# Kernel optimization log

Measured on AMD Instinct MI355X. Metric: run time of the kernel, lower is better.

## Reference

```python
import jax, jax.numpy as jnp
import numpy as np

C, FF, NH = 128, 2048, 8
B, D, H, W = 1, 16, 16, 16
EPS = 1e-5

def setup_inputs() -> dict:
    key = jax.random.key(0)
    ks = jax.random.split(key, 20)
    s = 0.02
    inp = {
        'x': jax.random.normal(ks[0], (B, C, D, H, W), jnp.float32),
        'Wq': jax.random.normal(ks[1], (C, C), jnp.float32) * s,
        'bq': jnp.zeros((C,), jnp.float32),
        'Wk': jax.random.normal(ks[2], (C, C), jnp.float32) * s,
        'bk': jnp.zeros((C,), jnp.float32),
        'Wv': jax.random.normal(ks[3], (C, C), jnp.float32) * s,
        'bv': jnp.zeros((C,), jnp.float32),
        'Wo': jax.random.normal(ks[4], (C, C), jnp.float32) * s,
        'bo': jnp.zeros((C,), jnp.float32),
        'W1': jax.random.normal(ks[5], (FF, C), jnp.float32) * s,
        'b1': jnp.zeros((FF,), jnp.float32),
        'W2': jax.random.normal(ks[6], (C, FF), jnp.float32) * s,
        'b2': jnp.zeros((C,), jnp.float32),
        'g1': jnp.ones((C,), jnp.float32),
        'be1': jnp.zeros((C,), jnp.float32),
        'g2': jnp.ones((C,), jnp.float32),
        'be2': jnp.zeros((C,), jnp.float32),
    }
    return inp

def _layernorm(t, g, b):
    # normalize over last (channel) dim, biased variance like torch LayerNorm
    m = jnp.mean(t, axis=-1, keepdims=True)
    v = jnp.mean(jnp.square(t - m), axis=-1, keepdims=True)
    return (t - m) * jax.lax.rsqrt(v + EPS) * g + b

def reference(x, Wq, bq, Wk, bk, Wv, bv, Wo, bo, W1, b1, W2, b2, g1, be1, g2, be2):
    b_, c, d, h, w = x.shape
    n = d * h * w
    hd = c // NH
    xf = x.reshape(b_, c, n)  # [B,C,N]
    # 1x1 conv3d == per-voxel linear over channels
    q = jnp.einsum('oc,bcn->bon', Wq, xf) + bq[:, None]
    k = jnp.einsum('oc,bcn->bon', Wk, xf) + bk[:, None]
    v = jnp.einsum('oc,bcn->bon', Wv, xf) + bv[:, None]
    q = q.reshape(b_, NH, hd, n)
    k = k.reshape(b_, NH, hd, n)
    v = v.reshape(b_, NH, hd, n)
    scores = jnp.einsum('bhcd,bhce->bhde', q, k) / (hd ** 0.5)  # [B,NH,N,N]
    probs = jax.nn.softmax(scores, axis=-1)
    attn = jnp.einsum('bhde,bhce->bhcd', probs, v).reshape(b_, c, n)
    attn = jnp.einsum('oc,bcn->bon', Wo, attn) + bo[:, None]
    x1 = xf + attn  # residual (dropout = identity at eval)
    x1 = _layernorm(x1.transpose(0, 2, 1), g1, be1)  # [B,N,C]
    hmid = jax.nn.relu(jnp.einsum('fc,bnc->bnf', W1, x1) + b1)
    ffn = jnp.einsum('cf,bnf->bnc', W2, hmid) + b2
    x2 = _layernorm(x1 + ffn, g2, be2)
    return x2.transpose(0, 2, 1).reshape(b_, c, d, h, w)
```

## Files before the change

### kernel.cpp

```cpp
#include <hip/hip_runtime.h>
#include <hip/hip_bf16.h>

typedef __hip_bfloat16 bf16;
typedef short short8 __attribute__((ext_vector_type(8)));
typedef float f32x4 __attribute__((ext_vector_type(4)));

#define C_   128
#define N_   4096
#define NH_  8
#define HD_  16
#define FF_  2048
#define SCALE_Q 0.360673760222241f

__device__ __forceinline__ unsigned short f2bf_bits(float f) {
    bf16 h = __float2bfloat16(f);
    return *reinterpret_cast<unsigned short*>(&h);
}
__device__ __forceinline__ unsigned int pack_trunc(float lo, float hi) {
    return (__float_as_uint(hi) & 0xffff0000u) | (__float_as_uint(lo) >> 16);
}
__device__ __forceinline__ short f2bf_trunc(float f) {
    return (short)(__float_as_uint(f) >> 16);
}
__device__ __forceinline__ float bfs2f(short s) {
    return __uint_as_float(((unsigned int)(unsigned short)s) << 16);
}
__device__ __forceinline__ float fast_exp2(float x) {
    return __builtin_amdgcn_exp2f(x);
}
__device__ __forceinline__ f32x4 mfma16(short8 a, short8 b, f32x4 c) {
    return __builtin_amdgcn_mfma_f32_16x16x32_bf16(a, b, c, 0, 0, 0);
}

__global__ void __launch_bounds__(256) k_prep(
    const float* __restrict__ Wq, const float* __restrict__ Wk,
    const float* __restrict__ Wv, const float* __restrict__ Wo,
    const float* __restrict__ W1, const float* __restrict__ W2,
    const float* __restrict__ x,
    bf16* __restrict__ Wqkvf, bf16* __restrict__ Wof,
    bf16* __restrict__ W1f, bf16* __restrict__ W2f,
    bf16* __restrict__ xTf)
{
    __shared__ float xs[4][512];
    const int tid = threadIdx.x, wave = tid >> 6, lane = tid & 63;
    const int gw = blockIdx.x * 4 + wave;
    const int q = lane >> 4;

    if (gw < 1152) {
        const float* src; bf16* dst; int K, otile, kch, blk;
        if (gw < 96)        { src = 0;  dst = Wqkvf; K = 128;  otile = gw >> 2;          kch = gw & 3;  blk = gw; }
        else if (gw < 128)  { int i = gw - 96;  src = Wo; dst = Wof;  K = 128;  otile = i >> 2; kch = i & 3;  blk = i; }
        else if (gw < 640)  { int i = gw - 128; src = W1; dst = W1f;  K = 128;  otile = i >> 2; kch = i & 3;  blk = i; }
        else                { int i = gw - 640; src = W2; dst = W2f;  K = 2048; otile = i >> 6; kch = i & 63; blk = i; }
        const int o = otile * 16 + (lane & 15);
        const int k0 = kch * 32 + 4 * q;
        const float* row;
        if (gw < 96) {
            row = (o < 128) ? (Wq + o * 128) : (o < 256) ? (Wk + (o - 128) * 128)
                                             : (Wv + (o - 256) * 128);
        } else {
            row = src + (size_t)o * K;
        }
        const float4 A = *(const float4*)(row + k0);
        const float4 B = *(const float4*)(row + k0 + 16);
        short8 v;
        v[0] = f2bf_bits(A.x); v[1] = f2bf_bits(B.x);
        v[2] = f2bf_bits(A.y); v[3] = f2bf_bits(B.y);
        v[4] = f2bf_bits(A.z); v[5] = f2bf_bits(B.z);
        v[6] = f2bf_bits(A.w); v[7] = f2bf_bits(B.w);
        *(short8*)((short*)dst + (size_t)blk * 512 + lane * 8) = v;
    } else {
        const int i = gw - 1152;
        const int n0 = (i >> 2) << 4, c0 = (i & 3) << 5;
        float* S = xs[wave];
        const int cl = lane & 31, ns = (lane >> 5) << 3;
        const float* p = x + (size_t)(c0 + cl) * N_ + n0 + ns;
        *(float4*)(S + cl * 16 + ns)     = *(const float4*)(p);
        *(float4*)(S + cl * 16 + ns + 4) = *(const float4*)(p + 4);
        short8 v;
        #pragma unroll
        for (int j = 0; j < 8; ++j) {
            const int ko = ((j & 1) << 4) + 4 * q + (j >> 1);
            v[j] = f2bf_bits(S[ko * 16 + (lane & 15)]);
        }
        *(short8*)((short*)xTf + (size_t)i * 512 + lane * 8) = v;
    }
}

__global__ void __launch_bounds__(256) k_qkv(
    const bf16* __restrict__ xTf, const bf16* __restrict__ Wqkvf,
    const float* __restrict__ bq, const float* __restrict__ bk, const float* __restrict__ bv,
    bf16* __restrict__ qf, bf16* __restrict__ kf, bf16* __restrict__ vf)
{
    __shared__ short tb[4][512];
    const int tid = threadIdx.x, wave = tid >> 6, lane = tid & 63;
    const int col = lane & 15, quad = lane >> 4;
    const int gw = blockIdx.x * 4 + wave;
    const int rt = gw / 24, ct = gw % 24;
    f32x4 acc = {};
    #pragma unroll
    for (int c = 0; c < 4; ++c) {
        short8 a = *(const short8*)(xTf + ((size_t)(rt * 4 + c) << 9) + lane * 8);
        short8 b = *(const short8*)(Wqkvf + ((size_t)(ct * 4 + c) << 9) + lane * 8);
        acc = mfma16(a, b, acc);
    }
    if (ct < 16) {
        short* T = tb[wave];
        const float bb = (ct < 8) ? bq[ct * 16 + col] : bk[(ct - 8) * 16 + col];
        const float sc = (ct < 8) ? SCALE_Q : 1.0f;
        #pragma unroll
        for (int r = 0; r < 4; ++r)
            T[(col >> 3) * 128 + (quad * 4 + r) * 8 + (col & 7)] =
                f2bf_trunc((acc[r] + bb) * sc);
        if (lane < 32) {
            short8 w = *(const short8*)(T + lane * 8);
            short* dst = (ct < 8) ? (short*)qf + ((ct << 8) + rt) * 256
                                  : (short*)kf + (((ct - 8) << 8) + rt) * 256;
            *(short8*)(dst + lane * 8) = w;
        }
    } else {
        const float bb = bv[(ct - 16) * 16 + col];
        short* vs = (short*)vf + ((((ct - 16) << 7) + (rt >> 1)) << 9);
        #pragma unroll
        for (int r = 0; r < 4; ++r) {
            const int local = quad * 4 + r;
            const int pos = local * 2 + (rt & 1);
            vs[((pos >> 3) * 16 + col) * 8 + (pos & 7)] = f2bf_trunc(acc[r] + bb);
        }
    }
}

__global__ void __launch_bounds__(256)
attn_kernel(const bf16* __restrict__ qf, const bf16* __restrict__ kf,
            const bf16* __restrict__ vf, bf16* __restrict__ af)
{
    __shared__ __align__(16) union {
        unsigned int P[4][2][320];
        float comb[4][64][8];
    } sh;
    const int tid = threadIdx.x, wave = tid >> 6, lane = tid & 63;
    const int col = lane & 15, quad = lane >> 4;
    const int gw = blockIdx.x;
    const int h  = gw >> 8;
    const int tile = gw & 255;
    const f32x4 zero = {};

    short8 aq = {};
    if (quad < 2)
        aq = *(const short8*)(qf + ((size_t)((h << 8) + tile) << 8) + lane * 8);

    f32x4 accO0 = {}, accO1 = {};
    float L[4] = {0.f, 0.f, 0.f, 0.f};

    const int kbeg = wave << 10;
    unsigned int* P0 = &sh.P[wave][0][0];
    unsigned int* P1 = &sh.P[wave][1][0];

    for (int i = 0; i < 32; i += 2) {
        const int mA = kbeg + (i << 5);
        const int mB = mA + 32;

        short8 bkA0 = {}, bkA1 = {}, bkB0 = {}, bkB1 = {};
        if (quad < 2) {
            const bf16* ka = kf + ((size_t)((h << 8) + (mA >> 4)) << 8) + lane * 8;
            bkA0 = *(const short8*)(ka);
            bkA1 = *(const short8*)(ka + 256);
            bkB0 = *(const short8*)(ka + 512);
            bkB1 = *(const short8*)(ka + 768);
        }
        f32x4 s0 = mfma16(aq, bkA0, zero);
        f32x4 s1 = mfma16(aq, bkA1, zero);
        f32x4 s2 = mfma16(aq, bkB0, zero);
        f32x4 s3 = mfma16(aq, bkB1, zero);
        #pragma unroll
        for (int r = 0; r < 4; ++r) {
            const float p0 = fast_exp2(s0[r]);
            const float p1 = fast_exp2(s1[r]);
            const float p2 = fast_exp2(s2[r]);
            const float p3 = fast_exp2(s3[r]);
            L[r] += (p0 + p1) + (p2 + p3);
            P0[(quad * 4 + r) * 20 + col] = pack_trunc(p0, p1);
            P1[(quad * 4 + r) * 20 + col] = pack_trunc(p2, p3);
        }
        short8 vA = *(const short8*)(vf + ((size_t)((h << 7) + (mA >> 5)) << 9) + lane * 8);
        short8 vB = *(const short8*)(vf + ((size_t)((h << 7) + (mB >> 5)) << 9) + lane * 8);
        short8 ap0 = *(const short8*)((const short*)P0 + col * 40 + quad * 8);
        accO0 = mfma16(ap0, vA, accO0);
        short8 ap1 = *(const short8*)((const short*)P1 + col * 40 + quad * 8);
        accO1 = mfma16(ap1, vB, accO1);
    }

    f32x4 accO;
    #pragma unroll
    for (int r = 0; r < 4; ++r) accO[r] = accO0[r] + accO1[r];

    __syncthreads();
    #pragma unroll
    for (int r = 0; r < 4; ++r) {
        sh.comb[wave][lane][r]     = accO[r];
        sh.comb[wave][lane][4 + r] = L[r];
    }
    __syncthreads();

    if (wave == 0) {
        #pragma unroll
        for (int r = 0; r < 4; ++r) {
            float O = sh.comb[0][lane][r] + sh.comb[1][lane][r]
                    + sh.comb[2][lane][r] + sh.comb[3][lane][r];
            float l = sh.comb[0][lane][4+r] + sh.comb[1][lane][4+r]
                    + sh.comb[2][lane][4+r] + sh.comb[3][lane][4+r];
            l += __shfl_xor(l, 1); l += __shfl_xor(l, 2);
            l += __shfl_xor(l, 4); l += __shfl_xor(l, 8);
            const int row16 = quad * 4 + r;
            const int pk = (col << 1) + (h & 1);
            af[((tile << 2) + (h >> 1)) * 512 + (((pk >> 3) << 4) + row16) * 8 + (pk & 7)] =
                __float2bfloat16(O / l);
        }
    }
}

__global__ void __launch_bounds__(256, 1)
k_mega(const bf16* __restrict__ af, const bf16* __restrict__ xTf,
       const bf16* __restrict__ Wof, const bf16* __restrict__ W1f, const bf16* __restrict__ W2f,
       const float* __restrict__ bo, const float* __restrict__ b1, const float* __restrict__ b2,
       const float* __restrict__ g1, const float* __restrict__ be1,
       const float* __restrict__ g2, const float* __restrict__ be2,
       float* __restrict__ out)
{
    __shared__ __align__(16) unsigned int Pb[4][2][320];
    __shared__ float comb[128][64];
    const int tid = threadIdx.x, wave = tid >> 6, lane = tid & 63;
    const int col = lane & 15, quad = lane >> 4;
    const int rt = blockIdx.x, n0 = rt << 4;
    const f32x4 zero = {};

    short8 ao[4], xt[4];
    #pragma unroll
    for (int c = 0; c < 4; ++c) {
        ao[c] = *(const short8*)(af  + ((size_t)(rt * 4 + c) << 9) + lane * 8);
        xt[c] = *(const short8*)(xTf + ((size_t)(rt * 4 + c) << 9) + lane * 8);
    }
    f32x4 d[8];
    #pragma unroll
    for (int t = 0; t < 8; ++t) d[t] = zero;
    short8 wa[4], wb[4];
    #pragma unroll
    for (int c = 0; c < 4; ++c)
        wa[c] = *(const short8*)(Wof + ((size_t)(c) << 9) + lane * 8);
    #pragma unroll
    for (int t = 0; t < 8; t += 2) {
        #pragma unroll
        for (int c = 0; c < 4; ++c)
            wb[c] = *(const short8*)(Wof + ((size_t)((t + 1) * 4 + c) << 9) + lane * 8);
        #pragma unroll
        for (int c = 0; c < 4; ++c) d[t] = mfma16(ao[c], wa[c], d[t]);
        if (t + 2 < 8) {
            #pragma unroll
            for (int c = 0; c < 4; ++c)
                wa[c] = *(const short8*)(Wof + ((size_t)((t + 2) * 4 + c) << 9) + lane * 8);
        }
        #pragma unroll
        for (int c = 0; c < 4; ++c) d[t + 1] = mfma16(ao[c], wb[c], d[t + 1]);
    }
    #pragma unroll
    for (int t = 0; t < 8; ++t) {
        const float bt = bo[t * 16 + col];
        #pragma unroll
        for (int r = 0; r < 4; ++r) d[t][r] += bt;
    }

    float x1f[4][8];
    #pragma unroll
    for (int c = 0; c < 4; ++c) {
        unsigned int* Pw = &Pb[wave][c & 1][0];
        const short* Ps = (const short*)Pw;
        #pragma unroll
        for (int r = 0; r < 4; ++r)
            Pw[(quad * 4 + r) * 20 + col] = pack_trunc(d[2 * c][r], d[2 * c + 1][r]);
        short8 ar = *(const short8*)(Ps + col * 40 + quad * 8);
        #pragma unroll
        for (int j = 0; j < 8; ++j)
            x1f[c][j] = bfs2f(ar[j]) + bfs2f(xt[c][j]);
    }

    float s = 0.f, ss = 0.f;
    #pragma unroll
    for (int c = 0; c < 4; ++c)
        #pragma unroll
        for (int j = 0; j < 8; ++j) { s += x1f[c][j]; ss += x1f[c][j] * x1f[c][j]; }
    s  += __shfl_xor(s, 16);  s  += __shfl_xor(s, 32);
    ss += __shfl_xor(ss, 16); ss += __shfl_xor(ss, 32);
    const float m1 = s * (1.f / 128.f);
    const float rstd1 = rsqrtf(ss * (1.f / 128.f) - m1 * m1 + 1e-5f);
    short8 aq1[4];
    #pragma unroll
    for (int c = 0; c < 4; ++c)
        #pragma unroll
        for (int j = 0; j < 8; ++j) {
            const int pos = quad * 8 + j;
            const int ko = ((pos & 1) << 4) + (pos >> 1);
            const int ch = c * 32 + ko;
            aq1[c][j] = f2bf_trunc((x1f[c][j] - m1) * rstd1 * g1[ch] + be1[ch]);
        }

    f32x4 ACC[8];
    #pragma unroll
    for (int t = 0; t < 8; ++t) ACC[t] = zero;
    const int fbase = wave << 4;
    short8 w1a[8], w2a[8], w1b[8], w2b[8];
    #pragma unroll
    for (int c = 0; c < 8; ++c) {
        w1a[c] = *(const short8*)(W1f + ((size_t)(fbase * 8 + c) << 9) + lane * 8);
        w2a[c] = *(const short8*)(W2f + ((size_t)(c * 64 + fbase) << 9) + lane * 8);
    }
    for (int i = 0; i < 16; i += 2) {
        const int f0 = fbase + i, f1 = f0 + 1;
        #pragma unroll
        for (int c = 0; c < 8; ++c) {
            w1b[c] = *(const short8*)(W1f + ((size_t)(f1 * 8 + c) << 9) + lane * 8);
            w2b[c] = *(const short8*)(W2f + ((size_t)(c * 64 + f1) << 9) + lane * 8);
        }
        {
            f32x4 p0 = zero, p1 = zero;
            #pragma unroll
            for (int c = 0; c < 4; ++c) p0 = mfma16(aq1[c], w1a[c], p0);
            #pragma unroll
            for (int c = 0; c < 4; ++c) p1 = mfma16(aq1[c], w1a[4 + c], p1);
            const float bb0 = b1[f0 * 32 + col], bb1 = b1[f0 * 32 + 16 + col];
            unsigned int* Pw = &Pb[wave][0][0];
            #pragma unroll
            for (int r = 0; r < 4; ++r)
                Pw[(quad * 4 + r) * 20 + col] =
                    pack_trunc(fmaxf(p0[r] + bb0, 0.f), fmaxf(p1[r] + bb1, 0.f));
            short8 ah = *(const short8*)((const short*)Pw + col * 40 + quad * 8);
            #pragma unroll
            for (int t = 0; t < 8; ++t) ACC[t] = mfma16(ah, w2a[t], ACC[t]);
        }
        if (i + 2 < 16) {
            const int f2 = f0 + 2;
            #pragma unroll
            for (int c = 0; c < 8; ++c) {
                w1a[c] = *(const short8*)(W1f + ((size_t)(f2 * 8 + c) << 9) + lane * 8);
                w2a[c] = *(const short8*)(W2f + ((size_t)(c * 64 + f2) << 9) + lane * 8);
            }
        }
        {
            f32x4 p0 = zero, p1 = zero;
            #pragma unroll
            for (int c = 0; c < 4; ++c) p0 = mfma16(aq1[c], w1b[c], p0);
            #pragma unroll
            for (int c = 0; c < 4; ++c) p1 = mfma16(aq1[c], w1b[4 + c], p1);
            const float bb0 = b1[f1 * 32 + col], bb1 = b1[f1 * 32 + 16 + col];
            unsigned int* Pw = &Pb[wave][1][0];
            #pragma unroll
            for (int r = 0; r < 4; ++r)
                Pw[(quad * 4 + r) * 20 + col] =
                    pack_trunc(fmaxf(p0[r] + bb0, 0.f), fmaxf(p1[r] + bb1, 0.f));
            short8 ah = *(const short8*)((const short*)Pw + col * 40 + quad * 8);
            #pragma unroll
            for (int t = 0; t < 8; ++t) ACC[t] = mfma16(ah, w2b[t], ACC[t]);
        }
    }

    #pragma unroll
    for (int t = 0; t < 8; ++t)
        #pragma unroll
        for (int r = 0; r < 4; ++r)
            comb[wave * 32 + t * 4 + r][lane] = ACC[t][r];
    if (wave == 0) {
        short* xb = (short*)&Pb[0][0][0];
        #pragma unroll
        for (int c = 0; c < 4; ++c)
            *(short8*)(xb + (col * 4 + c) * 32 + quad * 8) = aq1[c];
    }
    __syncthreads();

    {
        const short* xb = (const short*)&Pb[0][0][0];
        float t2[8][4];
        #pragma unroll
        for (int t = 0; t < 8; ++t) {
            const int ch = t * 16 + col;
            const int pk = (col << 1) + (t & 1);
            const int c = t >> 1;
            const float bb = b2[ch];
            #pragma unroll
            for (int r = 0; r < 4; ++r)
                t2[t][r] = comb[t * 4 + r][lane] + comb[32 + t * 4 + r][lane]
                         + comb[64 + t * 4 + r][lane] + comb[96 + t * 4 + r][lane]
                         + bb + bfs2f(xb[((quad * 4 + r) * 4 + c) * 32 + pk]);
        }
        #pragma unroll
        for (int r = 0; r < 4; ++r) {
            float S = 0.f, SS = 0.f;
            #pragma unroll
            for (int t = 0; t < 8; ++t) { S += t2[t][r]; SS += t2[t][r] * t2[t][r]; }
            S  += __shfl_xor(S, 1);  S  += __shfl_xor(S, 2);
            S  += __shfl_xor(S, 4);  S  += __shfl_xor(S, 8);
            SS += __shfl_xor(SS, 1); SS += __shfl_xor(SS, 2);
            SS += __shfl_xor(SS, 4); SS += __shfl_xor(SS, 8);
            const float m2 = S * (1.f / 128.f);
            const float rstd2 = rsqrtf(SS * (1.f / 128.f) - m2 * m2 + 1e-5f);
            #pragma unroll
            for (int tt = 0; tt < 2; ++tt) {
                const int t = wave * 2 + tt;
                const int ch = t * 16 + col;
                out[(size_t)ch * N_ + n0 + quad * 4 + r] =
                    (t2[t][r] - m2) * rstd2 * g2[ch] + be2[ch];
            }
        }
    }
}

extern "C" void kernel_launch(void* const* d_in, const int* in_sizes, int n_in,
                              void* d_out, int out_size, void* d_ws, size_t ws_size,
                              hipStream_t stream) {
    const float* x   = (const float*)d_in[0];
    const float* Wq  = (const float*)d_in[1];
    const float* bq  = (const float*)d_in[2];
    const float* Wk  = (const float*)d_in[3];
    const float* bk  = (const float*)d_in[4];
    const float* Wv  = (const float*)d_in[5];
    const float* bv  = (const float*)d_in[6];
    const float* Wo  = (const float*)d_in[7];
    const float* bo  = (const float*)d_in[8];
    const float* W1  = (const float*)d_in[9];
    const float* b1  = (const float*)d_in[10];
    const float* W2  = (const float*)d_in[11];
    const float* b2  = (const float*)d_in[12];
    const float* g1  = (const float*)d_in[13];
    const float* be1 = (const float*)d_in[14];
    const float* g2  = (const float*)d_in[15];
    const float* be2 = (const float*)d_in[16];
    float* out = (float*)d_out;

    char* ws = (char*)d_ws;
    bf16* xTf   = (bf16*)(ws + 0);
    bf16* qf    = (bf16*)(ws + 1048576);
    bf16* kf    = (bf16*)(ws + 2097152);
    bf16* vf    = (bf16*)(ws + 3145728);
    bf16* af    = (bf16*)(ws + 4194304);
    bf16* Wqkvf = (bf16*)(ws + 5242880);
    bf16* Wof   = (bf16*)(ws + 5341184);
    bf16* W1f   = (bf16*)(ws + 5373952);
    bf16* W2f   = (bf16*)(ws + 5898240);

    k_prep<<<544, 256, 0, stream>>>(Wq, Wk, Wv, Wo, W1, W2, x, Wqkvf, Wof, W1f, W2f, xTf);
    k_qkv<<<1536, 256, 0, stream>>>(xTf, Wqkvf, bq, bk, bv, qf, kf, vf);
    attn_kernel<<<2048, 256, 0, stream>>>(qf, kf, vf, af);
    k_mega<<<256, 256, 0, stream>>>(af, xTf, Wof, W1f, W2f, bo, b1, b2,
                                    g1, be1, g2, be2, out);
}
```

Baseline: 144.8 us.

## Process two query tiles per attention block to reuse K/V loads

Each attention block now handles two 16-row query tiles instead of one. Each K and V fragment loaded from global memory is used for both tiles, which halves K/V global traffic per query, and the grid shrinks from 2048 to 1024 blocks. The P scratch buffer is double-buffered by iteration parity, and two waves now finish the cross-wave combine instead of one. In exchange, each wave holds more registers and LDS, and there are half as many blocks to spread across CUs.

```diff
diff --git a/kernel.cpp b/kernel.cpp
--- a/kernel.cpp
+++ b/kernel.cpp
@@ -135,85 +135,85 @@
             const bf16* __restrict__ vf, bf16* __restrict__ af)
 {
     __shared__ __align__(16) union {
-        unsigned int P[4][2][320];
-        float comb[4][64][8];
+        unsigned int P[4][4][320];
+        float comb[4][64][16];
     } sh;
     const int tid = threadIdx.x, wave = tid >> 6, lane = tid & 63;
     const int col = lane & 15, quad = lane >> 4;
     const int gw = blockIdx.x;
-    const int h  = gw >> 8;
-    const int tile = gw & 255;
+    const int h  = gw >> 7;
+    const int tp = gw & 127;
+    const int t0 = tp << 1, t1 = t0 + 1;
     const f32x4 zero = {};
 
-    short8 aq = {};
-    if (quad < 2)
-        aq = *(const short8*)(qf + ((size_t)((h << 8) + tile) << 8) + lane * 8);
+    short8 aq0 = {}, aq1 = {};
+    if (quad < 2) {
+        aq0 = *(const short8*)(qf + ((size_t)((h << 8) + t0) << 8) + lane * 8);
+        aq1 = *(const short8*)(qf + ((size_t)((h << 8) + t1) << 8) + lane * 8);
+    }
 
     f32x4 accO0 = {}, accO1 = {};
-    float L[4] = {0.f, 0.f, 0.f, 0.f};
+    float L0[4] = {0.f, 0.f, 0.f, 0.f};
+    float L1[4] = {0.f, 0.f, 0.f, 0.f};
 
     const int kbeg = wave << 10;
-    unsigned int* P0 = &sh.P[wave][0][0];
-    unsigned int* P1 = &sh.P[wave][1][0];
-
-    for (int i = 0; i < 32; i += 2) {
-        const int mA = kbeg + (i << 5);
-        const int mB = mA + 32;
-
-        short8 bkA0 = {}, bkA1 = {}, bkB0 = {}, bkB1 = {};
+    for (int i = 0; i < 32; ++i) {
+        const int m0 = kbeg + (i << 5);
+        unsigned int* Pa = &sh.P[wave][(i & 1)][0];
+        unsigned int* Pb = &sh.P[wave][2 + (i & 1)][0];
+
+        short8 bk0 = {}, bk1 = {};
         if (quad < 2) {
-            const bf16* ka = kf + ((size_t)((h << 8) + (mA >> 4)) << 8) + lane * 8;
-            bkA0 = *(const short8*)(ka);
-            bkA1 = *(const short8*)(ka + 256);
-            bkB0 = *(const short8*)(ka + 512);
-            bkB1 = *(const short8*)(ka + 768);
-        }
-        f32x4 s0 = mfma16(aq, bkA0, zero);
-        f32x4 s1 = mfma16(aq, bkA1, zero);
-        f32x4 s2 = mfma16(aq, bkB0, zero);
-        f32x4 s3 = mfma16(aq, bkB1, zero);
+            const bf16* ka = kf + ((size_t)((h << 8) + (m0 >> 4)) << 8) + lane * 8;
+            bk0 = *(const short8*)(ka);
+            bk1 = *(const short8*)(ka + 256);
+        }
+        f32x4 sa0 = mfma16(aq0, bk0, zero);
+        f32x4 sa1 = mfma16(aq0, bk1, zero);
+        f32x4 sb0 = mfma16(aq1, bk0, zero);
+        f32x4 sb1 = mfma16(aq1, bk1, zero);
         #pragma unroll
         for (int r = 0; r < 4; ++r) {
-            const float p0 = fast_exp2(s0[r]);
-            const float p1 = fast_exp2(s1[r]);
-            const float p2 = fast_exp2(s2[r]);
-            const float p3 = fast_exp2(s3[r]);
-            L[r] += (p0 + p1) + (p2 + p3);
-            P0[(quad * 4 + r) * 20 + col] = pack_trunc(p0, p1);
-            P1[(quad * 4 + r) * 20 + col] = pack_trunc(p2, p3);
-        }
-        short8 vA = *(const short8*)(vf + ((size_t)((h << 7) + (mA >> 5)) << 9) + lane * 8);
-        short8 vB = *(const short8*)(vf + ((size_t)((h << 7) + (mB >> 5)) << 9) + lane * 8);
-        short8 ap0 = *(const short8*)((const short*)P0 + col * 40 + quad * 8);
+            const float p0 = fast_exp2(sa0[r]);
+            const float p1 = fast_exp2(sa1[r]);
+            const float p2 = fast_exp2(sb0[r]);
+            const float p3 = fast_exp2(sb1[r]);
+            L0[r] += p0 + p1;
+            L1[r] += p2 + p3;
+            Pa[(quad * 4 + r) * 20 + col] = pack_trunc(p0, p1);
+            Pb[(quad * 4 + r) * 20 + col] = pack_trunc(p2, p3);
+        }
+        short8 vA = *(const short8*)(vf + ((size_t)((h << 7) + (m0 >> 5)) << 9) + lane * 8);
+        short8 ap0 = *(const short8*)((const short*)Pa + col * 40 + quad * 8);
         accO0 = mfma16(ap0, vA, accO0);
-        short8 ap1 = *(const short8*)((const short*)P1 + col * 40 + quad * 8);
-        accO1 = mfma16(ap1, vB, accO1);
-    }
-
-    f32x4 accO;
-    #pragma unroll
-    for (int r = 0; r < 4; ++r) accO[r] = accO0[r] + accO1[r];
+        short8 ap1 = *(const short8*)((const short*)Pb + col * 40 + quad * 8);
+        accO1 = mfma16(ap1, vA, accO1);
+    }
 
     __syncthreads();
     #pragma unroll
     for (int r = 0; r < 4; ++r) {
-        sh.comb[wave][lane][r]     = accO[r];
-        sh.comb[wave][lane][4 + r] = L[r];
+        sh.comb[wave][lane][r]      = accO0[r];
+        sh.comb[wave][lane][4 + r]  = L0[r];
+        sh.comb[wave][lane][8 + r]  = accO1[r];
+        sh.comb[wave][lane][12 + r] = L1[r];
     }
     __syncthreads();
 
-    if (wave == 0) {
+    if (wave < 2) {
+        const int off = wave * 8;
+        const int tt = (wave == 0) ? t0 : t1;
         #pragma unroll
         for (int r = 0; r < 4; ++r) {
-            float O = sh.comb[0][lane][r] + sh.comb[1][lane][r]
-                    + sh.comb[2][lane][r] + sh.comb[3][lane][r];
-            float l = sh.comb[0][lane][4+r] + sh.comb[1][lane][4+r]
-                    + sh.comb[2][lane][4+r] + sh.comb[3][lane][4+r];
+            float O = sh.comb[0][lane][off + r] + sh.comb[1][lane][off + r]
+                    + sh.comb[2][lane][off + r] + sh.comb[3][lane][off + r];
+            float l = sh.comb[0][lane][off + 4 + r] + sh.comb[1][lane][off + 4 + r]
+                    + sh.comb[2][lane][off + 4 + r] + sh.comb[3][lane][off + 4 + r];
             l += __shfl_xor(l, 1); l += __shfl_xor(l, 2);
             l += __shfl_xor(l, 4); l += __shfl_xor(l, 8);
             const int row16 = quad * 4 + r;
             const int pk = (col << 1) + (h & 1);
-            af[((tile << 2) + (h >> 1)) * 512 + (((pk >> 3) << 4) + row16) * 8 + (pk & 7)] =
+            af[((tt << 2) + (h >> 1)) * 512 + (((pk >> 3) << 4) + row16) * 8 + (pk & 7)] =
                 __float2bfloat16(O / l);
         }
     }
@@ -447,7 +447,7 @@
 
     k_prep<<<544, 256, 0, stream>>>(Wq, Wk, Wv, Wo, W1, W2, x, Wqkvf, Wof, W1f, W2f, xTf);
     k_qkv<<<1536, 256, 0, stream>>>(xTf, Wqkvf, bq, bk, bv, qf, kf, vf);
-    attn_kernel<<<2048, 256, 0, stream>>>(qf, kf, vf, af);
+    attn_kernel<<<1024, 256, 0, stream>>>(qf, kf, vf, af);
     k_mega<<<256, 256, 0, stream>>>(af, xTf, Wof, W1f, W2f, bo, b1, b2,
                                     g1, be1, g2, be2, out);
 }
```

Result: no change. 144.0 us (-0.5%).
